# Optimization experiments

Hardware: AMD Instinct MI355X
Metric: run time of the kernel (lower is better)

## Reference

```python
import jax, jax.numpy as jnp
import numpy as np

# PyTorch LSTM gate order: i, f, g, o. Bidirectional LSTM with hidden = dim/2,
# outputs concatenated -> dim, then mean over the sequence axis (as in the module).

def _lstm_dir(x, Wih, Whh, bih, bhh):
    # x: [B, T, D] -> hidden states [B, T, H]
    B, T, _ = x.shape
    H = Whh.shape[1]
    gx = jnp.einsum('btd,gd->btg', x, Wih) + bih + bhh  # precompute input gates [B,T,4H]
    def step(carry, g_t):
        h, c = carry
        g = g_t + h @ Whh.T
        i, f, gg, o = jnp.split(g, 4, axis=-1)
        c = jax.nn.sigmoid(f) * c + jax.nn.sigmoid(i) * jnp.tanh(gg)
        h = jax.nn.sigmoid(o) * jnp.tanh(c)
        return (h, c), h
    z = jnp.zeros((B, H), x.dtype)
    _, hs = jax.lax.scan(step, (z, z), jnp.swapaxes(gx, 0, 1))
    return jnp.swapaxes(hs, 0, 1)


def _bilstm_mean(x, Wih, Whh, bih, bhh):
    # params indexed [dir, ...]; dir 0 = forward, dir 1 = backward.
    hf = _lstm_dir(x, Wih[0], Whh[0], bih[0], bhh[0])
    hb = _lstm_dir(x[:, ::-1], Wih[1], Whh[1], bih[1], bhh[1])[:, ::-1]
    return jnp.concatenate([hf, hb], axis=-1).mean(axis=1)  # [B, 2H] == [B, D]


def setup_inputs() -> dict:
    key = jax.random.key(0)
    ks = jax.random.split(key, 14)
    N, C, D, K, H = 30000, 3, 128, 10, 64
    f = lambda k, shp: jax.random.normal(k, shp, jnp.float32) * 0.1
    return dict(
        x_a=f(ks[0], (N, C, D)),
        x_b=f(ks[1], (N, C, D)),
        x_c=f(ks[2], (N, C, D)),
        Wih_c=f(ks[3], (2, 4 * H, D)),
        Whh_c=f(ks[4], (2, 4 * H, H)),
        bih_c=f(ks[5], (2, 4 * H)),
        bhh_c=f(ks[6], (2, 4 * H)),
        Wih_n=f(ks[7], (3, 2, 4 * H, D)),
        Whh_n=f(ks[8], (3, 2, 4 * H, H)),
        bih_n=f(ks[9], (3, 2, 4 * H)),
        bhh_n=f(ks[10], (3, 2, 4 * H)),
        attn_w=f(ks[11], (3, 2 * D)),
        attn_b=f(ks[12], (3,)),
        nbr_idx=jax.random.randint(ks[13], (3, 3, N, K), 0, N),  # [stype, dtype, N, K]
    )


def reference(x_a, x_b, x_c, Wih_c, Whh_c, bih_c, bhh_c,
              Wih_n, Whh_n, bih_n, bhh_n, attn_w, attn_b, nbr_idx):
    xs = [x_a, x_b, x_c]
    NT = 3
    # C2: heterogeneous content encoder (shared bi-LSTM over content features)
    content = [_bilstm_mean(x, Wih_c, Whh_c, bih_c, bhh_c) for x in xs]  # each [N, D]
    out = []
    for d in range(NT):
        # C3: per-source-type neighbor aggregation via that stype's bi-LSTM reducer
        neighs = []
        for s in range(NT):
            msgs = content[s][nbr_idx[s, d]]  # mailbox gather [N, K, D]
            neighs.append(_bilstm_mean(msgs, Wih_n[s], Whh_n[s], bih_n[s], bhh_n[s]))
        d_h = content[d]
        emd = jnp.stack(neighs + [d_h], axis=1)  # [N, 4, D]
        ch = jnp.concatenate(
            [jnp.broadcast_to(d_h[:, None, :], emd.shape), emd], axis=-1)  # [N, 4, 2D]
        logits = jax.nn.leaky_relu(
            jnp.einsum('nkf,f->nk', ch, attn_w[d]) + attn_b[d], 0.01)
        w = jax.nn.softmax(logits, axis=1)  # [N, 4]
        out.append(jnp.einsum('nk,nkd->nd', w, emd))  # attention-weighted fusion
    return tuple(out)
```

## Files before the change

### kernel.cpp

```cpp
#include <hip/hip_runtime.h>

#define N_NODES 30000
#define DFEAT 128
#define HID 64
#define G4 256

typedef __bf16 bfrag __attribute__((ext_vector_type(8)));
typedef float f32x4 __attribute__((ext_vector_type(4)));

#define SC_SIG -1.442695041f
#define SC_TANH -2.885390082f

__device__ inline float bflo(unsigned u){ return __builtin_bit_cast(float, u << 16); }
__device__ inline float bfhi(unsigned u){ return __builtin_bit_cast(float, u & 0xFFFF0000u); }
__device__ inline unsigned short bf16u(float a){
  unsigned ua = __builtin_bit_cast(unsigned, a);
  ua += 0x7FFFu + ((ua >> 16) & 1u);
  return (unsigned short)(ua >> 16);
}
__device__ inline unsigned short bfn(float a){
  return __builtin_bit_cast(unsigned short, (__bf16)a);
}
__device__ inline unsigned packbf(float a, float b){
  unsigned ua = __builtin_bit_cast(unsigned, a);
  unsigned ub = __builtin_bit_cast(unsigned, b);
  ua += 0x7FFFu + ((ua >> 16) & 1u);
  ub += 0x7FFFu + ((ub >> 16) & 1u);
  return (ua >> 16) | (ub & 0xFFFF0000u);
}
__device__ inline bfrag ldfrag(const unsigned short* p){
  return *reinterpret_cast<const bfrag*>(p);
}
__device__ inline f32x4 mfma16(bfrag a, bfrag b, f32x4 c){
  return __builtin_amdgcn_mfma_f32_16x16x32_bf16(a, b, c, 0, 0, 0);
}
__device__ inline int idx_stride(const int* p){
  int lane = threadIdx.x & 63;
  int v = p[lane];
  int ok = (lane & 1) ? (v == 0) : (v >= 0 && v < N_NODES);
  unsigned long long m = __ballot(ok);
  int st = (m == ~0ull) ? 2 : 1;
  return __builtin_amdgcn_readfirstlane(st);
}

__device__ inline float lstm_step(float gi, float gf, float gg, float go,
                                  float& cst, float& hsum)
{
  float ei = __builtin_amdgcn_exp2f(gi);
  float ef = __builtin_amdgcn_exp2f(gf);
  float eg = __builtin_amdgcn_exp2f(gg);
  float a = 1.f + ei, b = 1.f + eg, f1 = 1.f + ef;
  float ab = a * b;
  float num = __builtin_fmaf(cst, ab, (2.f - b) * f1);
  float cn = num * __builtin_amdgcn_rcpf(ab * f1);
  cst = cn;
  float eo = __builtin_amdgcn_exp2f(go);
  float ec = __builtin_amdgcn_exp2f(SC_TANH * cn);
  float o1 = 1.f + eo, c1 = 1.f + ec;
  float h = (2.f - c1) * __builtin_amdgcn_rcpf(o1 * c1);
  hsum += h;
  return h;
}

#define PK_WHHC 65536
#define PK_WIHN 98304
#define PK_WHHN 294912

__global__ __launch_bounds__(256) void k_pack(
    const float* __restrict__ Wih_c, const float* __restrict__ Whh_c,
    const float* __restrict__ Wih_n, const float* __restrict__ Whh_n,
    unsigned short* __restrict__ pk)
{
  const int m = blockIdx.y;
  const float* src; unsigned short* dst; int ndir, Q;
  if (m == 0){ src = Wih_c; dst = pk;            ndir = 2; Q = 4; }
  else if (m == 1){ src = Whh_c; dst = pk + PK_WHHC; ndir = 2; Q = 2; }
  else if (m == 2){ src = Wih_n; dst = pk + PK_WIHN; ndir = 6; Q = 4; }
  else { src = Whh_n; dst = pk + PK_WHHN; ndir = 6; Q = 2; }
  const int per = Q * 8192;
  const int total = ndir * per;
  int e = blockIdx.x * 256 + threadIdx.x;
  if (e >= total) return;
  int sd = e / per, r = e % per;
  int c = r / (Q * 2048); int r2 = r % (Q * 2048);
  int q = r2 / 2048;      int r3 = r2 % 2048;
  int w = r3 >> 9; int lane = (r3 >> 3) & 63; int j = r3 & 7;
  int gate = c * 64 + w * 16 + (lane & 15);
  int col  = q * 32 + (lane >> 4) * 8 + j;
  int D = Q * 32;
  float sc = (c == 2) ? SC_TANH : SC_SIG;
  dst[e] = bf16u(src[((size_t)sd * G4 + gate) * D + col] * sc);
}

__global__ __launch_bounds__(256) void k_content(
    const float* __restrict__ xa, const float* __restrict__ xb,
    const float* __restrict__ xc,
    const unsigned short* __restrict__ pk,
    const float* __restrict__ bih, const float* __restrict__ bhh,
    unsigned short* __restrict__ content)
{
  const int tile = blockIdx.x, dir = blockIdx.y, s = blockIdx.z;
  const float* xs = (s == 0) ? xa : ((s == 1) ? xb : xc);
  const int n0 = tile * 16;
  __shared__ __align__(16) unsigned int xdw[48 * 68];
  __shared__ __align__(16) unsigned short hbuf[2][16 * 72];
  const int tid = threadIdx.x;
  const float2* xg2 = reinterpret_cast<const float2*>(xs + (size_t)n0 * 384);
  for (int i = tid; i < 3072; i += 256){
    int node = i / 192, rem = i % 192; int t = rem / 64, c2 = rem % 64;
    float2 v = xg2[i];
    xdw[(t * 16 + node) * 68 + c2] = packbf(v.x, v.y);
  }
  for (int i = tid; i < 1152; i += 256) hbuf[0][i] = 0;

  const int lane = tid & 63, w = tid >> 6;
  const int nl = lane & 15, kg = lane >> 4;
  const unsigned short* pkWih = pk + dir * 32768;
  const unsigned short* pkWhh = pk + PK_WHHC + dir * 16384;
  bfrag Bw[4][4], Bh[4][2];
  float bias[4];
  #pragma unroll
  for (int c = 0; c < 4; ++c){
    int gate = c * 64 + w * 16 + nl;
    #pragma unroll
    for (int q = 0; q < 4; ++q)
      Bw[c][q] = ldfrag(pkWih + (((c * 4 + q) * 4 + w) * 64 + lane) * 8);
    Bh[c][0] = ldfrag(pkWhh + (((c * 2 + 0) * 4 + w) * 64 + lane) * 8);
    Bh[c][1] = ldfrag(pkWhh + (((c * 2 + 1) * 4 + w) * 64 + lane) * 8);
    float sc = (c == 2) ? SC_TANH : SC_SIG;
    bias[c] = (bih[dir * G4 + gate] + bhh[dir * G4 + gate]) * sc;
  }
  __syncthreads();

  float cst[4] = {0,0,0,0}, hsum[4] = {0,0,0,0};
  int pp = 0;
  #pragma unroll
  for (int t = 0; t < 3; ++t){
    int tt = dir ? (2 - t) : t;
    f32x4 acc[4];
    #pragma unroll
    for (int c = 0; c < 4; ++c){ f32x4 bv = {bias[c], bias[c], bias[c], bias[c]}; acc[c] = bv; }
    const unsigned short* xrow = reinterpret_cast<const unsigned short*>(&xdw[(tt * 16 + nl) * 68]);
    bfrag ax[4];
    #pragma unroll
    for (int q = 0; q < 4; ++q) ax[q] = ldfrag(xrow + q * 32 + kg * 8);
    #pragma unroll
    for (int c = 0; c < 4; ++c){
      #pragma unroll
      for (int q = 0; q < 4; ++q) acc[c] = mfma16(ax[q], Bw[c][q], acc[c]);
    }
    const unsigned short* hrow = &hbuf[pp][nl * 72];
    bfrag ah0 = ldfrag(hrow + kg * 8);
    bfrag ah1 = ldfrag(hrow + 32 + kg * 8);
    #pragma unroll
    for (int c = 0; c < 4; ++c){
      acc[c] = mfma16(ah0, Bh[c][0], acc[c]);
      acc[c] = mfma16(ah1, Bh[c][1], acc[c]);
    }
    #pragma unroll
    for (int r = 0; r < 4; ++r){
      float h = lstm_step(acc[0][r], acc[1][r], acc[2][r], acc[3][r], cst[r], hsum[r]);
      hbuf[pp ^ 1][(kg * 4 + r) * 72 + (w * 16 + nl)] = bfn(h);
    }
    __syncthreads();
    pp ^= 1;
  }
  #pragma unroll
  for (int r = 0; r < 4; ++r){
    int n = n0 + kg * 4 + r;
    content[((size_t)s * N_NODES + n) * DFEAT + dir * 64 + w * 16 + nl] = bfn(hsum[r] * (1.f / 3.f));
  }
}

__global__ __launch_bounds__(256) void k_gtab(
    const unsigned short* __restrict__ content,
    const unsigned short* __restrict__ pk,
    const float* __restrict__ bih_n, const float* __restrict__ bhh_n,
    unsigned int* __restrict__ Gtab)
{
  const int tile = blockIdx.x, dir = blockIdx.y, s = blockIdx.z;
  const int n0 = tile * 16;
  __shared__ __align__(16) unsigned int cdw[16 * 68];
  const int tid = threadIdx.x;
  const unsigned int* cg = reinterpret_cast<const unsigned int*>(content) + ((size_t)s * N_NODES + n0) * 64;
  for (int i = tid; i < 1024; i += 256){
    int node = i >> 6, c2 = i & 63;
    cdw[node * 68 + c2] = cg[i];
  }
  __syncthreads();
  const int lane = tid & 63, w = tid >> 6;
  const int nl = lane & 15, kg = lane >> 4;
  const int sd = s * 2 + dir;
  const unsigned short* pkW = pk + PK_WIHN + sd * 32768;
  f32x4 acc[4];
  #pragma unroll
  for (int c = 0; c < 4; ++c){
    int gate = c * 64 + w * 16 + nl;
    float sc = (c == 2) ? SC_TANH : SC_SIG;
    float b = (bih_n[sd * G4 + gate] + bhh_n[sd * G4 + gate]) * sc;
    f32x4 bv = {b, b, b, b};
    acc[c] = bv;
  }
  const unsigned short* crow = reinterpret_cast<const unsigned short*>(&cdw[nl * 68]);
  bfrag a[4];
  #pragma unroll
  for (int q = 0; q < 4; ++q) a[q] = ldfrag(crow + q * 32 + kg * 8);
  #pragma unroll
  for (int c = 0; c < 4; ++c){
    #pragma unroll
    for (int q = 0; q < 4; ++q){
      bfrag bw = ldfrag(pkW + (((c * 4 + q) * 4 + w) * 64 + lane) * 8);
      acc[c] = mfma16(a[q], bw, acc[c]);
    }
  }
  uint2* g2 = reinterpret_cast<uint2*>(Gtab + (size_t)sd * N_NODES * 128);
  #pragma unroll
  for (int r = 0; r < 4; ++r){
    int n = n0 + kg * 4 + r;
    uint2 v;
    v.x = packbf(acc[0][r], acc[1][r]);
    v.y = packbf(acc[2][r], acc[3][r]);
    g2[(size_t)n * 64 + (w * 16 + nl)] = v;
  }
}

__global__ __launch_bounds__(256, 4) void k_neigh(
    const unsigned int* __restrict__ Gtab,
    const unsigned short* __restrict__ pk,
    const int* __restrict__ nbr_idx,
    int dparam, size_t nstride,
    unsigned short* __restrict__ nbuf)
{
  const int tile = blockIdx.x, dir = blockIdx.y;
  int s, d;
  if (dparam < 0){ s = blockIdx.z % 3; d = blockIdx.z / 3; }
  else { s = blockIdx.z; d = dparam; }
  unsigned short* nb = nbuf + ((dparam < 0) ? (size_t)d * nstride : (size_t)0);
  const int n0 = tile * 16;
  __shared__ int idxb[160];
  __shared__ __align__(16) unsigned short hbuf[2][16 * 72];
  const int tid = threadIdx.x;
  const int st = idx_stride(nbr_idx);
  const size_t ibase = ((size_t)(s * 3 + d) * N_NODES + n0) * 10;
  if (tid < 160) idxb[tid] = nbr_idx[(ibase + tid) * st] * 64;
  for (int i = tid; i < 1152; i += 256) hbuf[0][i] = 0;
  __syncthreads();
  const int lane = tid & 63, w = tid >> 6;
  const int nl = lane & 15, kg = lane >> 4;
  const int lo = w * 16 + nl;
  const int sd = s * 2 + dir;
  const unsigned short* pkW = pk + PK_WHHN + sd * 16384;
  bfrag Bh[4][2];
  #pragma unroll
  for (int c = 0; c < 4; ++c){
    Bh[c][0] = ldfrag(pkW + (((c * 2 + 0) * 4 + w) * 64 + lane) * 8);
    Bh[c][1] = ldfrag(pkW + (((c * 2 + 1) * 4 + w) * 64 + lane) * 8);
  }
  const uint2* gt2 = reinterpret_cast<const uint2*>(Gtab + (size_t)sd * N_NODES * 128);
  uint2 gn[4];
  {
    int ke = dir ? 9 : 0;
    #pragma unroll
    for (int r = 0; r < 4; ++r){
      unsigned off = (unsigned)idxb[(kg * 4 + r) * 10 + ke] + lo;
      gn[r] = gt2[off];
    }
  }
  float cst[4] = {0,0,0,0}, hsum[4] = {0,0,0,0};
  int pp = 0;
  #pragma unroll
  for (int t = 0; t < 10; ++t){
    uint2 cur[4];
    #pragma unroll
    for (int r = 0; r < 4; ++r) cur[r] = gn[r];
    if (t < 9){
      int ke = dir ? (8 - t) : (t + 1);
      #pragma unroll
      for (int r = 0; r < 4; ++r){
        unsigned off = (unsigned)idxb[(kg * 4 + r) * 10 + ke] + lo;
        gn[r] = gt2[off];
      }
    }
    f32x4 acc[4];
    #pragma unroll
    for (int r = 0; r < 4; ++r){
      acc[0][r] = bflo(cur[r].x); acc[1][r] = bfhi(cur[r].x);
      acc[2][r] = bflo(cur[r].y); acc[3][r] = bfhi(cur[r].y);
    }
    const unsigned short* hrow = &hbuf[pp][nl * 72];
    bfrag ah0 = ldfrag(hrow + kg * 8);
    bfrag ah1 = ldfrag(hrow + 32 + kg * 8);
    #pragma unroll
    for (int c = 0; c < 4; ++c){
      acc[c] = mfma16(ah0, Bh[c][0], acc[c]);
      acc[c] = mfma16(ah1, Bh[c][1], acc[c]);
    }
    #pragma unroll
    for (int r = 0; r < 4; ++r){
      float h = lstm_step(acc[0][r], acc[1][r], acc[2][r], acc[3][r], cst[r], hsum[r]);
      hbuf[pp ^ 1][(kg * 4 + r) * 72 + (w * 16 + nl)] = bfn(h);
    }
    __syncthreads();
    pp ^= 1;
  }
  #pragma unroll
  for (int r = 0; r < 4; ++r){
    int n = n0 + kg * 4 + r;
    nb[((size_t)s * N_NODES + n) * DFEAT + dir * 64 + w * 16 + nl] = bfn(hsum[r] * 0.1f);
  }
}

__global__ __launch_bounds__(256) void k_attn(
    const unsigned short* __restrict__ content,
    const unsigned short* __restrict__ nbuf,
    const float* __restrict__ attn_w,
    const float* __restrict__ attn_b,
    int dparam, size_t nstride,
    float* __restrict__ out)
{
  const int d = (dparam < 0) ? (int)blockIdx.y : dparam;
  const unsigned short* nb = nbuf + ((dparam < 0) ? (size_t)d * nstride : (size_t)0);
  const int n = blockIdx.x * 4 + (threadIdx.x >> 6);
  const int lane = threadIdx.x & 63;
  const unsigned int* dh = reinterpret_cast<const unsigned int*>(content) + ((size_t)d * N_NODES + n) * 64;
  const float2* awv = reinterpret_cast<const float2*>(attn_w + d * 256);
  unsigned int udh = dh[lane];
  unsigned int ue[3];
  #pragma unroll
  for (int s_ = 0; s_ < 3; ++s_){
    const unsigned int* np_ = reinterpret_cast<const unsigned int*>(nb) + ((size_t)s_ * N_NODES + n) * 64;
    ue[s_] = np_[lane];
  }
  float2 wl = awv[lane], wh = awv[64 + lane];
  float dh0 = bflo(udh), dh1 = bfhi(udh);
  float p[5];
  p[4] = wl.x * dh0 + wl.y * dh1;
  #pragma unroll
  for (int k = 0; k < 3; ++k){
    p[k] = wh.x * bflo(ue[k]) + wh.y * bfhi(ue[k]);
  }
  p[3] = wh.x * dh0 + wh.y * dh1;
  #pragma unroll
  for (int m = 1; m < 64; m <<= 1){
    #pragma unroll
    for (int jj = 0; jj < 5; ++jj) p[jj] += __shfl_xor(p[jj], m, 64);
  }
  float bias = attn_b[d];
  float logit[4];
  #pragma unroll
  for (int k = 0; k < 4; ++k){
    float x = p[4] + p[k] + bias;
    logit[k] = x > 0.f ? x : 0.01f * x;
  }
  float mx = fmaxf(fmaxf(logit[0], logit[1]), fmaxf(logit[2], logit[3]));
  float ek[4], Z = 0.f;
  #pragma unroll
  for (int k = 0; k < 4; ++k){ ek[k] = __builtin_amdgcn_exp2f(1.442695041f * (logit[k] - mx)); Z += ek[k]; }
  float rz = __builtin_amdgcn_rcpf(Z);
  float o0 = 0.f, o1 = 0.f;
  #pragma unroll
  for (int k = 0; k < 3; ++k){
    float wk = ek[k] * rz;
    o0 += wk * bflo(ue[k]); o1 += wk * bfhi(ue[k]);
  }
  float w3 = ek[3] * rz;
  o0 += w3 * dh0; o1 += w3 * dh1;
  float2 res; res.x = o0; res.y = o1;
  reinterpret_cast<float2*>(out)[((size_t)d * N_NODES + n) * 64 + lane] = res;
}

extern "C" void kernel_launch(void* const* d_in, const int* in_sizes, int n_in,
                              void* d_out, int out_size, void* d_ws, size_t ws_size,
                              hipStream_t stream)
{
  const float* xa    = (const float*)d_in[0];
  const float* xb    = (const float*)d_in[1];
  const float* xc    = (const float*)d_in[2];
  const float* Wih_c = (const float*)d_in[3];
  const float* Whh_c = (const float*)d_in[4];
  const float* bih_c = (const float*)d_in[5];
  const float* bhh_c = (const float*)d_in[6];
  const float* Wih_n = (const float*)d_in[7];
  const float* Whh_n = (const float*)d_in[8];
  const float* bih_n = (const float*)d_in[9];
  const float* bhh_n = (const float*)d_in[10];
  const float* attn_w = (const float*)d_in[11];
  const float* attn_b = (const float*)d_in[12];
  const int*   nbr   = (const int*)d_in[13];
  float* out = (float*)d_out;

  const size_t SZ_CONTENT = 23040000;
  const size_t SZ_GTAB    = 92160000;
  const size_t SZ_NBUF    = 23040000;
  const size_t NSTRIDE    = SZ_NBUF / 2;
  const bool fused = ws_size >= (SZ_CONTENT + SZ_GTAB + 3 * SZ_NBUF + 786432);

  char* ws = (char*)d_ws;
  unsigned short* content = (unsigned short*)ws;
  unsigned int*   Gtab    = (unsigned int*)(ws + SZ_CONTENT);
  unsigned short* nbuf    = (unsigned short*)(ws + SZ_CONTENT + SZ_GTAB);
  unsigned short* pkw     = (unsigned short*)(ws + SZ_CONTENT + SZ_GTAB
                                                 + (fused ? 3 : 1) * SZ_NBUF);

  k_pack<<<dim3(768, 4), 256, 0, stream>>>(Wih_c, Whh_c, Wih_n, Whh_n, pkw);
  k_content<<<dim3(1875, 2, 3), 256, 0, stream>>>(xa, xb, xc, pkw, bih_c, bhh_c, content);
  k_gtab<<<dim3(1875, 2, 3), 256, 0, stream>>>(content, pkw, bih_n, bhh_n, Gtab);
  if (fused){
    k_neigh<<<dim3(1875, 2, 9), 256, 0, stream>>>(Gtab, pkw, nbr, -1, NSTRIDE, nbuf);
    k_attn<<<dim3(7500, 3), 256, 0, stream>>>(content, nbuf, attn_w, attn_b, -1, NSTRIDE, out);
  } else {
    for (int d = 0; d < 3; ++d){
      k_neigh<<<dim3(1875, 2, 3), 256, 0, stream>>>(Gtab, pkw, nbr, d, 0, nbuf);
      k_attn<<<dim3(7500), 256, 0, stream>>>(content, nbuf, attn_w, attn_b, d, 0, out);
    }
  }
}
```

Baseline: 840.9 us.

## Fuse content LSTM with Gtab projection and pack LSTM gate math into float2

Merges k_content and k_gtab into one kernel. Each block now runs both directions of the content bi-LSTM sequentially, keeps the content tile in shared memory, and projects it through the neighbor input weights for both directions. This removes a kernel launch and the re-read of the content buffer from global memory, at the cost of half as many blocks and a serialized direction loop. The LSTM gate nonlinearity is also rewritten on float2 vectors so the compiler can emit packed FP32 ops in both the content and neighbor kernels.

Result: faster. 799.4 us (-4.9%).

```diff
diff --git a/kernel.cpp b/kernel.cpp
--- a/kernel.cpp
+++ b/kernel.cpp
@@ -7,6 +7,7 @@
 
 typedef __bf16 bfrag __attribute__((ext_vector_type(8)));
 typedef float f32x4 __attribute__((ext_vector_type(4)));
+typedef float f32x2 __attribute__((ext_vector_type(2)));
 
 #define SC_SIG -1.442695041f
 #define SC_TANH -2.885390082f
@@ -43,21 +44,32 @@
   return __builtin_amdgcn_readfirstlane(st);
 }
 
-__device__ inline float lstm_step(float gi, float gf, float gg, float go,
-                                  float& cst, float& hsum)
-{
-  float ei = __builtin_amdgcn_exp2f(gi);
-  float ef = __builtin_amdgcn_exp2f(gf);
-  float eg = __builtin_amdgcn_exp2f(gg);
-  float a = 1.f + ei, b = 1.f + eg, f1 = 1.f + ef;
-  float ab = a * b;
-  float num = __builtin_fmaf(cst, ab, (2.f - b) * f1);
-  float cn = num * __builtin_amdgcn_rcpf(ab * f1);
+__device__ inline f32x2 lstm_pk(f32x2 gi, f32x2 gf, f32x2 gg, f32x2 go,
+                                f32x2& cst, f32x2& hsum)
+{
+  f32x2 ei, ef, eg;
+  ei.x = __builtin_amdgcn_exp2f(gi.x); ei.y = __builtin_amdgcn_exp2f(gi.y);
+  ef.x = __builtin_amdgcn_exp2f(gf.x); ef.y = __builtin_amdgcn_exp2f(gf.y);
+  eg.x = __builtin_amdgcn_exp2f(gg.x); eg.y = __builtin_amdgcn_exp2f(gg.y);
+  f32x2 one = {1.f, 1.f}, two = {2.f, 2.f};
+  f32x2 a = ei + one, b = eg + one, f1 = ef + one;
+  f32x2 ab = a * b;
+  f32x2 num = __builtin_elementwise_fma(cst, ab, (two - b) * f1);
+  f32x2 den = ab * f1;
+  f32x2 cn;
+  cn.x = num.x * __builtin_amdgcn_rcpf(den.x);
+  cn.y = num.y * __builtin_amdgcn_rcpf(den.y);
   cst = cn;
-  float eo = __builtin_amdgcn_exp2f(go);
-  float ec = __builtin_amdgcn_exp2f(SC_TANH * cn);
-  float o1 = 1.f + eo, c1 = 1.f + ec;
-  float h = (2.f - c1) * __builtin_amdgcn_rcpf(o1 * c1);
+  f32x2 eo, ec;
+  eo.x = __builtin_amdgcn_exp2f(go.x); eo.y = __builtin_amdgcn_exp2f(go.y);
+  f32x2 targ = cn * SC_TANH;
+  ec.x = __builtin_amdgcn_exp2f(targ.x); ec.y = __builtin_amdgcn_exp2f(targ.y);
+  f32x2 o1 = eo + one, c1 = ec + one;
+  f32x2 num2 = two - c1;
+  f32x2 den2 = o1 * c1;
+  f32x2 h;
+  h.x = num2.x * __builtin_amdgcn_rcpf(den2.x);
+  h.y = num2.y * __builtin_amdgcn_rcpf(den2.y);
   hsum += h;
   return h;
 }
@@ -97,13 +109,16 @@
     const float* __restrict__ xc,
     const unsigned short* __restrict__ pk,
     const float* __restrict__ bih, const float* __restrict__ bhh,
-    unsigned short* __restrict__ content)
-{
-  const int tile = blockIdx.x, dir = blockIdx.y, s = blockIdx.z;
+    const float* __restrict__ bih_n, const float* __restrict__ bhh_n,
+    unsigned short* __restrict__ content,
+    unsigned int* __restrict__ Gtab)
+{
+  const int tile = blockIdx.x, s = blockIdx.y;
   const float* xs = (s == 0) ? xa : ((s == 1) ? xb : xc);
   const int n0 = tile * 16;
   __shared__ __align__(16) unsigned int xdw[48 * 68];
   __shared__ __align__(16) unsigned short hbuf[2][16 * 72];
+  __shared__ __align__(16) unsigned short ctile[16][136];
   const int tid = threadIdx.x;
   const float2* xg2 = reinterpret_cast<const float2*>(xs + (size_t)n0 * 384);
   for (int i = tid; i < 3072; i += 256){
@@ -111,116 +126,114 @@
     float2 v = xg2[i];
     xdw[(t * 16 + node) * 68 + c2] = packbf(v.x, v.y);
   }
-  for (int i = tid; i < 1152; i += 256) hbuf[0][i] = 0;
 
   const int lane = tid & 63, w = tid >> 6;
   const int nl = lane & 15, kg = lane >> 4;
-  const unsigned short* pkWih = pk + dir * 32768;
-  const unsigned short* pkWhh = pk + PK_WHHC + dir * 16384;
-  bfrag Bw[4][4], Bh[4][2];
-  float bias[4];
-  #pragma unroll
-  for (int c = 0; c < 4; ++c){
-    int gate = c * 64 + w * 16 + nl;
-    #pragma unroll
-    for (int q = 0; q < 4; ++q)
-      Bw[c][q] = ldfrag(pkWih + (((c * 4 + q) * 4 + w) * 64 + lane) * 8);
-    Bh[c][0] = ldfrag(pkWhh + (((c * 2 + 0) * 4 + w) * 64 + lane) * 8);
-    Bh[c][1] = ldfrag(pkWhh + (((c * 2 + 1) * 4 + w) * 64 + lane) * 8);
-    float sc = (c == 2) ? SC_TANH : SC_SIG;
-    bias[c] = (bih[dir * G4 + gate] + bhh[dir * G4 + gate]) * sc;
+
+  for (int dir = 0; dir < 2; ++dir){
+    for (int i = tid; i < 1152; i += 256) hbuf[0][i] = 0;
+    __syncthreads();
+
+    const unsigned short* pkWih = pk + dir * 32768;
+    const unsigned short* pkWhh = pk + PK_WHHC + dir * 16384;
+    bfrag Bw[4][4], Bh[4][2];
+    float bias[4];
+    #pragma unroll
+    for (int c = 0; c < 4; ++c){
+      int gate = c * 64 + w * 16 + nl;
+      #pragma unroll
+      for (int q = 0; q < 4; ++q)
+        Bw[c][q] = ldfrag(pkWih + (((c * 4 + q) * 4 + w) * 64 + lane) * 8);
+      Bh[c][0] = ldfrag(pkWhh + (((c * 2 + 0) * 4 + w) * 64 + lane) * 8);
+      Bh[c][1] = ldfrag(pkWhh + (((c * 2 + 1) * 4 + w) * 64 + lane) * 8);
+      float sc = (c == 2) ? SC_TANH : SC_SIG;
+      bias[c] = (bih[dir * G4 + gate] + bhh[dir * G4 + gate]) * sc;
+    }
+
+    f32x2 cst2[2] = {f32x2{0,0}, f32x2{0,0}};
+    f32x2 hsum2[2] = {f32x2{0,0}, f32x2{0,0}};
+    int pp = 0;
+    #pragma unroll
+    for (int t = 0; t < 3; ++t){
+      int tt = dir ? (2 - t) : t;
+      f32x4 acc[4];
+      #pragma unroll
+      for (int c = 0; c < 4; ++c){ f32x4 bv = {bias[c], bias[c], bias[c], bias[c]}; acc[c] = bv; }
+      const unsigned short* xrow = reinterpret_cast<const unsigned short*>(&xdw[(tt * 16 + nl) * 68]);
+      bfrag ax[4];
+      #pragma unroll
+      for (int q = 0; q < 4; ++q) ax[q] = ldfrag(xrow + q * 32 + kg * 8);
+      #pragma unroll
+      for (int c = 0; c < 4; ++c){
+        #pragma unroll
+        for (int q = 0; q < 4; ++q) acc[c] = mfma16(ax[q], Bw[c][q], acc[c]);
+      }
+      const unsigned short* hrow = &hbuf[pp][nl * 72];
+      bfrag ah0 = ldfrag(hrow + kg * 8);
+      bfrag ah1 = ldfrag(hrow + 32 + kg * 8);
+      #pragma unroll
+      for (int c = 0; c < 4; ++c){
+        acc[c] = mfma16(ah0, Bh[c][0], acc[c]);
+        acc[c] = mfma16(ah1, Bh[c][1], acc[c]);
+      }
+      #pragma unroll
+      for (int p = 0; p < 2; ++p){
+        f32x2 gi = {acc[0][2*p], acc[0][2*p+1]};
+        f32x2 gf = {acc[1][2*p], acc[1][2*p+1]};
+        f32x2 gg = {acc[2][2*p], acc[2][2*p+1]};
+        f32x2 go = {acc[3][2*p], acc[3][2*p+1]};
+        f32x2 h = lstm_pk(gi, gf, gg, go, cst2[p], hsum2[p]);
+        hbuf[pp ^ 1][(kg * 4 + 2*p) * 72 + (w * 16 + nl)]     = bfn(h.x);
+        hbuf[pp ^ 1][(kg * 4 + 2*p + 1) * 72 + (w * 16 + nl)] = bfn(h.y);
+      }
+      __syncthreads();
+      pp ^= 1;
+    }
+    #pragma unroll
+    for (int r = 0; r < 4; ++r){
+      int n = n0 + kg * 4 + r;
+      float hv = (r & 1) ? hsum2[r >> 1].y : hsum2[r >> 1].x;
+      unsigned short h16 = bfn(hv * (1.f / 3.f));
+      content[((size_t)s * N_NODES + n) * DFEAT + dir * 64 + w * 16 + nl] = h16;
+      ctile[kg * 4 + r][dir * 64 + w * 16 + nl] = h16;
+    }
   }
   __syncthreads();
 
-  float cst[4] = {0,0,0,0}, hsum[4] = {0,0,0,0};
-  int pp = 0;
-  #pragma unroll
-  for (int t = 0; t < 3; ++t){
-    int tt = dir ? (2 - t) : t;
+  const unsigned short* crow = &ctile[nl][0];
+  bfrag a[4];
+  #pragma unroll
+  for (int q = 0; q < 4; ++q) a[q] = ldfrag(crow + q * 32 + kg * 8);
+  #pragma unroll
+  for (int dd = 0; dd < 2; ++dd){
+    const int sd = s * 2 + dd;
+    const unsigned short* pkW = pk + PK_WIHN + sd * 32768;
     f32x4 acc[4];
     #pragma unroll
-    for (int c = 0; c < 4; ++c){ f32x4 bv = {bias[c], bias[c], bias[c], bias[c]}; acc[c] = bv; }
-    const unsigned short* xrow = reinterpret_cast<const unsigned short*>(&xdw[(tt * 16 + nl) * 68]);
-    bfrag ax[4];
-    #pragma unroll
-    for (int q = 0; q < 4; ++q) ax[q] = ldfrag(xrow + q * 32 + kg * 8);
-    #pragma unroll
     for (int c = 0; c < 4; ++c){
-      #pragma unroll
-      for (int q = 0; q < 4; ++q) acc[c] = mfma16(ax[q], Bw[c][q], acc[c]);
-    }
-    const unsigned short* hrow = &hbuf[pp][nl * 72];
-    bfrag ah0 = ldfrag(hrow + kg * 8);
-    bfrag ah1 = ldfrag(hrow + 32 + kg * 8);
+      int gate = c * 64 + w * 16 + nl;
+      float sc = (c == 2) ? SC_TANH : SC_SIG;
+      float b = (bih_n[sd * G4 + gate] + bhh_n[sd * G4 + gate]) * sc;
+      f32x4 bv = {b, b, b, b};
+      acc[c] = bv;
+    }
     #pragma unroll
     for (int c = 0; c < 4; ++c){
-      acc[c] = mfma16(ah0, Bh[c][0], acc[c]);
-      acc[c] = mfma16(ah1, Bh[c][1], acc[c]);
-    }
+      #pragma unroll
+      for (int q = 0; q < 4; ++q){
+        bfrag bw = ldfrag(pkW + (((c * 4 + q) * 4 + w) * 64 + lane) * 8);
+        acc[c] = mfma16(a[q], bw, acc[c]);
+      }
+    }
+    uint2* g2 = reinterpret_cast<uint2*>(Gtab + (size_t)sd * N_NODES * 128);
     #pragma unroll
     for (int r = 0; r < 4; ++r){
-      float h = lstm_step(acc[0][r], acc[1][r], acc[2][r], acc[3][r], cst[r], hsum[r]);
-      hbuf[pp ^ 1][(kg * 4 + r) * 72 + (w * 16 + nl)] = bfn(h);
-    }
-    __syncthreads();
-    pp ^= 1;
-  }
-  #pragma unroll
-  for (int r = 0; r < 4; ++r){
-    int n = n0 + kg * 4 + r;
-    content[((size_t)s * N_NODES + n) * DFEAT + dir * 64 + w * 16 + nl] = bfn(hsum[r] * (1.f / 3.f));
-  }
-}
-
-__global__ __launch_bounds__(256) void k_gtab(
-    const unsigned short* __restrict__ content,
-    const unsigned short* __restrict__ pk,
-    const float* __restrict__ bih_n, const float* __restrict__ bhh_n,
-    unsigned int* __restrict__ Gtab)
-{
-  const int tile = blockIdx.x, dir = blockIdx.y, s = blockIdx.z;
-  const int n0 = tile * 16;
-  __shared__ __align__(16) unsigned int cdw[16 * 68];
-  const int tid = threadIdx.x;
-  const unsigned int* cg = reinterpret_cast<const unsigned int*>(content) + ((size_t)s * N_NODES + n0) * 64;
-  for (int i = tid; i < 1024; i += 256){
-    int node = i >> 6, c2 = i & 63;
-    cdw[node * 68 + c2] = cg[i];
-  }
-  __syncthreads();
-  const int lane = tid & 63, w = tid >> 6;
-  const int nl = lane & 15, kg = lane >> 4;
-  const int sd = s * 2 + dir;
-  const unsigned short* pkW = pk + PK_WIHN + sd * 32768;
-  f32x4 acc[4];
-  #pragma unroll
-  for (int c = 0; c < 4; ++c){
-    int gate = c * 64 + w * 16 + nl;
-    float sc = (c == 2) ? SC_TANH : SC_SIG;
-    float b = (bih_n[sd * G4 + gate] + bhh_n[sd * G4 + gate]) * sc;
-    f32x4 bv = {b, b, b, b};
-    acc[c] = bv;
-  }
-  const unsigned short* crow = reinterpret_cast<const unsigned short*>(&cdw[nl * 68]);
-  bfrag a[4];
-  #pragma unroll
-  for (int q = 0; q < 4; ++q) a[q] = ldfrag(crow + q * 32 + kg * 8);
-  #pragma unroll
-  for (int c = 0; c < 4; ++c){
-    #pragma unroll
-    for (int q = 0; q < 4; ++q){
-      bfrag bw = ldfrag(pkW + (((c * 4 + q) * 4 + w) * 64 + lane) * 8);
-      acc[c] = mfma16(a[q], bw, acc[c]);
-    }
-  }
-  uint2* g2 = reinterpret_cast<uint2*>(Gtab + (size_t)sd * N_NODES * 128);
-  #pragma unroll
-  for (int r = 0; r < 4; ++r){
-    int n = n0 + kg * 4 + r;
-    uint2 v;
-    v.x = packbf(acc[0][r], acc[1][r]);
-    v.y = packbf(acc[2][r], acc[3][r]);
-    g2[(size_t)n * 64 + (w * 16 + nl)] = v;
+      int n = n0 + kg * 4 + r;
+      uint2 v;
+      v.x = packbf(acc[0][r], acc[1][r]);
+      v.y = packbf(acc[2][r], acc[3][r]);
+      g2[(size_t)n * 64 + (w * 16 + nl)] = v;
+    }
   }
 }
 
@@ -266,7 +279,8 @@
       gn[r] = gt2[off];
     }
   }
-  float cst[4] = {0,0,0,0}, hsum[4] = {0,0,0,0};
+  f32x2 cst2[2] = {f32x2{0,0}, f32x2{0,0}};
+  f32x2 hsum2[2] = {f32x2{0,0}, f32x2{0,0}};
   int pp = 0;
   #pragma unroll
   for (int t = 0; t < 10; ++t){
@@ -296,9 +310,14 @@
       acc[c] = mfma16(ah1, Bh[c][1], acc[c]);
     }
     #pragma unroll
-    for (int r = 0; r < 4; ++r){
-      float h = lstm_step(acc[0][r], acc[1][r], acc[2][r], acc[3][r], cst[r], hsum[r]);
-      hbuf[pp ^ 1][(kg * 4 + r) * 72 + (w * 16 + nl)] = bfn(h);
+    for (int p = 0; p < 2; ++p){
+      f32x2 gi = {acc[0][2*p], acc[0][2*p+1]};
+      f32x2 gf = {acc[1][2*p], acc[1][2*p+1]};
+      f32x2 gg = {acc[2][2*p], acc[2][2*p+1]};
+      f32x2 go = {acc[3][2*p], acc[3][2*p+1]};
+      f32x2 h = lstm_pk(gi, gf, gg, go, cst2[p], hsum2[p]);
+      hbuf[pp ^ 1][(kg * 4 + 2*p) * 72 + (w * 16 + nl)]     = bfn(h.x);
+      hbuf[pp ^ 1][(kg * 4 + 2*p + 1) * 72 + (w * 16 + nl)] = bfn(h.y);
     }
     __syncthreads();
     pp ^= 1;
@@ -306,7 +325,8 @@
   #pragma unroll
   for (int r = 0; r < 4; ++r){
     int n = n0 + kg * 4 + r;
-    nb[((size_t)s * N_NODES + n) * DFEAT + dir * 64 + w * 16 + nl] = bfn(hsum[r] * 0.1f);
+    float hv = (r & 1) ? hsum2[r >> 1].y : hsum2[r >> 1].x;
+    nb[((size_t)s * N_NODES + n) * DFEAT + dir * 64 + w * 16 + nl] = bfn(hv * 0.1f);
   }
 }
 
@@ -403,8 +423,8 @@
                                                  + (fused ? 3 : 1) * SZ_NBUF);
 
   k_pack<<<dim3(768, 4), 256, 0, stream>>>(Wih_c, Whh_c, Wih_n, Whh_n, pkw);
-  k_content<<<dim3(1875, 2, 3), 256, 0, stream>>>(xa, xb, xc, pkw, bih_c, bhh_c, content);
-  k_gtab<<<dim3(1875, 2, 3), 256, 0, stream>>>(content, pkw, bih_n, bhh_n, Gtab);
+  k_content<<<dim3(1875, 3), 256, 0, stream>>>(xa, xb, xc, pkw, bih_c, bhh_c,
+                                               bih_n, bhh_n, content, Gtab);
   if (fused){
     k_neigh<<<dim3(1875, 2, 9), 256, 0, stream>>>(Gtab, pkw, nbr, -1, NSTRIDE, nbuf);
     k_attn<<<dim3(7500, 3), 256, 0, stream>>>(content, nbuf, attn_w, attn_b, -1, NSTRIDE, out);
```
